# Optimization experiments

Measured on AMD Instinct MI355X. Metric: run time of the kernel, lower is better.

## Reference

```python
import jax, jax.numpy as jnp
import numpy as np

H = 2048          # hidden_size
NH = 32           # num_attention_heads
NKV = 8           # num_key_value_heads
HD = H // NH      # head_dim = 64
ROT = int(HD * 0.25)  # rotary_ndims = 16
THETA = 10000.0


def _rope_cos_sin(seq_len, position_ids):
    # inv_freq over the rotary dims
    inv_freq = 1.0 / (THETA ** (jnp.arange(0, ROT, 2, dtype=jnp.float32) / ROT))
    t = jnp.arange(seq_len, dtype=jnp.float32)
    freqs = jnp.outer(t, inv_freq)              # [S, ROT/2]
    emb = jnp.concatenate([freqs, freqs], -1)   # [S, ROT]
    cos = jnp.cos(emb)[position_ids][:, None]   # [B, 1, Q, ROT]
    sin = jnp.sin(emb)[position_ids][:, None]
    return cos, sin


def _rotate_half(x):
    x1, x2 = jnp.split(x, 2, axis=-1)
    return jnp.concatenate([-x2, x1], axis=-1)


def setup_inputs() -> dict:
    key = jax.random.key(0)
    ks = jax.random.split(key, 5)
    B, S = 2, 2048
    hidden_states = jax.random.normal(ks[0], (B, S, H), jnp.float32)
    # additive causal mask
    neg = jnp.finfo(jnp.float32).min
    causal = jnp.where(jnp.tril(jnp.ones((S, S), bool)), 0.0, neg).astype(jnp.float32)
    attention_mask = jnp.broadcast_to(causal[None, None], (B, 1, S, S))
    position_ids = jnp.broadcast_to(jnp.arange(S, dtype=jnp.int32)[None], (B, S))
    sc = 0.02
    Wq = jax.random.normal(ks[1], (H, H), jnp.float32) * sc
    Wk = jax.random.normal(ks[2], (NKV * HD, H), jnp.float32) * sc
    Wv = jax.random.normal(ks[3], (NKV * HD, H), jnp.float32) * sc
    Wo = jax.random.normal(ks[4], (H, H), jnp.float32) * sc
    return {"hidden_states": hidden_states, "attention_mask": attention_mask,
            "position_ids": position_ids, "Wq": Wq, "Wk": Wk, "Wv": Wv, "Wo": Wo}


def reference(hidden_states, attention_mask, position_ids, Wq, Wk, Wv, Wo):
    B, S, _ = hidden_states.shape
    q = (hidden_states @ Wq.T).reshape(B, S, NH, HD).transpose(0, 2, 1, 3)    # [B,NH,S,HD]
    k = (hidden_states @ Wk.T).reshape(B, S, NKV, HD).transpose(0, 2, 1, 3)   # [B,NKV,S,HD]
    v = (hidden_states @ Wv.T).reshape(B, S, NKV, HD).transpose(0, 2, 1, 3)

    cos, sin = _rope_cos_sin(S, position_ids)  # [B,1,S,ROT]
    q_rot, q_pass = q[..., :ROT], q[..., ROT:]
    k_rot, k_pass = k[..., :ROT], k[..., ROT:]
    q_rot = q_rot * cos + _rotate_half(q_rot) * sin
    k_rot = k_rot * cos + _rotate_half(k_rot) * sin
    q = jnp.concatenate([q_rot, q_pass], -1)
    k = jnp.concatenate([k_rot, k_pass], -1)

    # GQA without materializing repeated K/V: group Q heads per KV head
    G = NH // NKV
    qg = q.reshape(B, NKV, G, S, HD)
    scores = jnp.einsum('bhgqd,bhkd->bhgqk', qg, k) / np.sqrt(HD)
    scores = scores.reshape(B, NH, S, S) + attention_mask
    probs = jax.nn.softmax(scores.astype(jnp.float32), axis=-1).astype(q.dtype)
    out = jnp.einsum('bhgqk,bhkd->bhgqd', probs.reshape(B, NKV, G, S, S), v)
    out = out.reshape(B, NH, S, HD).transpose(0, 2, 1, 3).reshape(B, S, H)
    return out @ Wo.T
```

## Files before the change

### kernel.cpp

```cpp
#include <hip/hip_runtime.h>

typedef unsigned short u16;
typedef short s16x8 __attribute__((ext_vector_type(8)));
typedef u16 u16x8 __attribute__((ext_vector_type(8)));
typedef u16 u16x4 __attribute__((ext_vector_type(4)));
typedef float f32x4 __attribute__((ext_vector_type(4)));
typedef __bf16 bf16x8 __attribute__((ext_vector_type(8)));
typedef __bf16 bf16x4 __attribute__((ext_vector_type(4)));

#define B_ 2
#define S_ 2048
#define H_ 2048
#define NH_ 32
#define NKV_ 8
#define HD_ 64
#define LDQ_ 3072
#define NTOK (B_ * S_)
#define SC_ 0.18033688011112042f

__device__ __forceinline__ u16 f2bf(float f) {
  unsigned u = __float_as_uint(f);
  u += 0x7fffu + ((u >> 16) & 1u);
  return (u16)(u >> 16);
}
__device__ __forceinline__ float bf2f(u16 h) {
  return __uint_as_float(((unsigned)h) << 16);
}

__device__ __forceinline__ void gload16(const void* g, void* l) {
  __builtin_amdgcn_global_load_lds(
      (const __attribute__((address_space(1))) unsigned int*)g,
      (__attribute__((address_space(3))) unsigned int*)l, 16, 0, 0);
}

__device__ __forceinline__ f32x4 mfma16(s16x8 a, s16x8 b, f32x4 c) {
  return __builtin_amdgcn_mfma_f32_16x16x32_bf16(
      __builtin_bit_cast(bf16x8, a), __builtin_bit_cast(bf16x8, b), c, 0, 0, 0);
}

__global__ __launch_bounds__(256) void cvt_all(const float* __restrict__ hs,
    const float* __restrict__ wq, const float* __restrict__ wk,
    const float* __restrict__ wv, const float* __restrict__ wo,
    u16* __restrict__ xbf, u16* __restrict__ wqkv, u16* __restrict__ wob,
    float* __restrict__ tab) {
  int i = blockIdx.x * 256 + threadIdx.x;
  if (i >= 2359296) {
    int t = i - 2359296;
    if (t < S_ * 8) {
      int p = t >> 3, k = t & 7;
      float inv = powf(10000.0f, -(float)k * 0.125f);
      float ang = (float)p * inv;
      tab[p * 16 + k] = cosf(ang);
      tab[p * 16 + 8 + k] = sinf(ang);
    }
    return;
  }
  const float* s; u16* d; int j;
  if (i < 1048576)      { s = hs; d = xbf;            j = i; }
  else if (i < 1572864) { s = wq; d = wqkv;           j = i - 1048576; }
  else if (i < 1703936) { s = wk; d = wqkv + 4194304; j = i - 1572864; }
  else if (i < 1835008) { s = wv; d = wqkv + 5242880; j = i - 1703936; }
  else                  { s = wo; d = wob;            j = i - 1835008; }
  const float4* sp = (const float4*)s + (size_t)j * 2;
  float4 a = sp[0], b = sp[1];
  u16x8 o;
  o[0] = f2bf(a.x); o[1] = f2bf(a.y); o[2] = f2bf(a.z); o[3] = f2bf(a.w);
  o[4] = f2bf(b.x); o[5] = f2bf(b.y); o[6] = f2bf(b.z); o[7] = f2bf(b.w);
  *((u16x8*)d + j) = o;
}

__device__ __forceinline__ void store_c(u16* p, float v) { *p = f2bf(v); }
__device__ __forceinline__ void store_c(float* p, float v) { *p = v; }

template <typename OutT, bool SCQ, bool ROPE, bool WRV>
__global__ __launch_bounds__(256, 3) void gemm_bt(const u16* __restrict__ A,
                                                  const u16* __restrict__ Bw,
                                                  OutT* __restrict__ C,
                                                  u16* __restrict__ Vt,
                                                  const float* __restrict__ tab,
                                                  int M, int N, int K) {
  __shared__ u16 lds[2 * 128 * 64];
  u16* ldsA = lds;
  u16* ldsB = lds + 128 * 64;
  const int tid = threadIdx.x;
  const int lane = tid & 63;
  const int wave = tid >> 6;
  const int wm = (wave & 1) * 64;
  const int wn = (wave >> 1) * 64;
  const int m0 = blockIdx.y * 128;
  const int n0 = blockIdx.x * 128;
  const int l15 = lane & 15;
  const int quad = lane >> 4;
  const int xs = l15 & 7;

  f32x4 acc[4][4];
#pragma unroll
  for (int i = 0; i < 4; ++i)
#pragma unroll
    for (int j = 0; j < 4; ++j) acc[i][j] = {0.f, 0.f, 0.f, 0.f};

  const u16* Ab = A + (size_t)m0 * K;
  const u16* Bb = Bw + (size_t)n0 * K;

  for (int k0 = 0; k0 < K; k0 += 64) {
    __syncthreads();
#pragma unroll
    for (int it = 0; it < 4; ++it) {
      int c = it * 256 + tid;
      int row = c >> 3;
      int sw = ((c & 7) ^ (row & 7)) * 8;
      gload16(Ab + (size_t)row * K + k0 + sw, ldsA + (size_t)c * 8);
      gload16(Bb + (size_t)row * K + k0 + sw, ldsB + (size_t)c * 8);
    }
    __syncthreads();
#pragma unroll
    for (int ks = 0; ks < 2; ++ks) {
      int slot = ((ks * 4 + quad) ^ xs) * 8;
      s16x8 af[4], bfr[4];
#pragma unroll
      for (int i = 0; i < 4; ++i)
        af[i] = *(const s16x8*)(ldsA + (size_t)(wm + i * 16 + l15) * 64 + slot);
#pragma unroll
      for (int j = 0; j < 4; ++j)
        bfr[j] = *(const s16x8*)(ldsB + (size_t)(wn + j * 16 + l15) * 64 + slot);
#pragma unroll
      for (int i = 0; i < 4; ++i)
#pragma unroll
        for (int j = 0; j < 4; ++j)
          acc[i][j] = mfma16(af[i], bfr[j], acc[i][j]);
    }
  }
  if (WRV && n0 >= 2560) {
#pragma unroll
    for (int i = 0; i < 4; ++i) {
      int row = m0 + wm + i * 16 + quad * 4;
      int bb = row >> 11;
      int s = row & (S_ - 1);
#pragma unroll
      for (int j = 0; j < 4; ++j) {
        int colb = n0 + wn + j * 16 - 2560;
        int kvh = colb >> 6;
        int d = (colb & 63) + l15;
        u16x4 w;
#pragma unroll
        for (int r = 0; r < 4; ++r) w[r] = f2bf(acc[i][j][r]);
        *(u16x4*)(Vt + ((size_t)(bb * 8 + kvh) * 64 + d) * (size_t)S_ + s) = w;
      }
    }
    return;
  }
  const float qs = (SCQ && n0 < 2048) ? SC_ : 1.0f;
  const bool doRope = ROPE && (n0 + wn < 2560);
#pragma unroll
  for (int i = 0; i < 4; ++i) {
    int row = m0 + wm + i * 16 + quad * 4;
#pragma unroll
    for (int j = 0; j < 4; ++j) {
      int col = n0 + wn + j * 16 + l15;
#pragma unroll
      for (int r = 0; r < 4; ++r) {
        float v = acc[i][j][r] * qs;
        if (ROPE) {
          if (j == 0 && doRope) {
            int p = (row + r) & (S_ - 1);
            float c = tab[p * 16 + (l15 & 7)];
            float s = tab[p * 16 + 8 + (l15 & 7)];
            float px = __shfl_xor(v, 8);
            v = (l15 < 8) ? (v * c - px * s) : (v * c + px * s);
          }
        }
        store_c(C + (size_t)(row + r) * N + col, v);
      }
    }
  }
}

template <bool DIAG>
__device__ __forceinline__ void softmax_pack(const f32x4* sc, u16* prow,
                                             int q2, int xs, int sb, int qg) {
#pragma unroll
  for (int nt = 0; nt < 4; ++nt) {
    f32x4 p;
#pragma unroll
    for (int r = 0; r < 4; ++r) {
      float e = __builtin_amdgcn_exp2f(sc[nt][r]);
      if (DIAG) e = (sb + nt * 16 + r > qg) ? 0.0f : e;
      p[r] = e;
    }
    bf16x4 w;
    w[0] = (__bf16)p[0]; w[1] = (__bf16)p[1];
    w[2] = (__bf16)p[2]; w[3] = (__bf16)p[3];
    *(bf16x4*)(prow + (((nt * 2) | q2) ^ xs) * 8) = w;
  }
}

__global__ __launch_bounds__(256, 3) void flash_attn(const u16* __restrict__ QKV,
                                                     const u16* __restrict__ Vt,
                                                     u16* __restrict__ O) {
  __shared__ u16 Kl2[2][64 * 64];
  __shared__ u16 Vl2[2][64 * 64];
  __shared__ u16 Pb[4][16 * 64];
  const int h = blockIdx.x;
  const int b = blockIdx.y;
  const int qt = 15 - (int)blockIdx.z;
  const int kvh = h >> 2;
  const int tid = threadIdx.x;
  const int lane = tid & 63;
  const int wave = tid >> 6;
  const int l15 = lane & 15;
  const int quad = lane >> 4;
  const int xs = l15 & 7;

  const u16* Qb = QKV + (size_t)b * S_ * LDQ_ + h * 64;
  const u16* Kb = QKV + (size_t)b * S_ * LDQ_ + 2048 + kvh * 64;
  const u16* Vb = Vt + (size_t)(b * 8 + kvh) * HD_ * S_;

  const int row0w = qt * 128 + wave * 32;

  s16x8 qf[2][2];
#pragma unroll
  for (int g = 0; g < 2; ++g) {
    int qrow = row0w + g * 16 + l15;
#pragma unroll
    for (int ks = 0; ks < 2; ++ks)
      qf[g][ks] = *(const s16x8*)(Qb + (size_t)qrow * LDQ_ + ks * 32 + quad * 8);
  }

  s16x8 ones;
#pragma unroll
  for (int i = 0; i < 8; ++i) ones[i] = (short)0x3F80;

  f32x4 acc_o[2][4];
#pragma unroll
  for (int g = 0; g < 2; ++g)
#pragma unroll
    for (int nt = 0; nt < 4; ++nt) acc_o[g][nt] = {0.f, 0.f, 0.f, 0.f};
  f32x4 acc_l[2] = {{0.f, 0.f, 0.f, 0.f}, {0.f, 0.f, 0.f, 0.f}};

  const int r0 = tid >> 3, c0 = tid & 7;
  const int ch0 = c0 * 8;
  const int r1 = r0 + 32;
  const int ss = (c0 ^ (r0 & 7)) * 8;

  const int nkt = 2 * qt + 2;

  u16* Pw = Pb[wave] + l15 * 64 + (quad & 1) * 4;
  const int q2 = quad >> 1;
  const u16* Pr0 = Pb[wave] + l15 * 64 + ((quad ^ xs) * 8);
  const u16* Pr1 = Pb[wave] + l15 * 64 + (((quad + 4) ^ xs) * 8);

  u16x8 kr0, kr1, vr0, vr1;
  kr0 = *(const u16x8*)(Kb + (size_t)r0 * LDQ_ + ch0);
  kr1 = *(const u16x8*)(Kb + (size_t)r1 * LDQ_ + ch0);
  vr0 = *(const u16x8*)(Vb + (size_t)r0 * S_ + ch0);
  vr1 = *(const u16x8*)(Vb + (size_t)r1 * S_ + ch0);

  for (int kt = 0; kt < nkt; ++kt) {
    u16* Kl = Kl2[kt & 1];
    u16* Vl = Vl2[kt & 1];
    *(u16x8*)(Kl + r0 * 64 + ss) = kr0;
    *(u16x8*)(Kl + r1 * 64 + ss) = kr1;
    *(u16x8*)(Vl + r0 * 64 + ss) = vr0;
    *(u16x8*)(Vl + r1 * 64 + ss) = vr1;
    __syncthreads();
    if (kt + 1 < nkt) {
      int kb = (kt + 1) * 64;
      kr0 = *(const u16x8*)(Kb + (size_t)(kb + r0) * LDQ_ + ch0);
      kr1 = *(const u16x8*)(Kb + (size_t)(kb + r1) * LDQ_ + ch0);
      vr0 = *(const u16x8*)(Vb + (size_t)r0 * S_ + kb + ch0);
      vr1 = *(const u16x8*)(Vb + (size_t)r1 * S_ + kb + ch0);
    }
    if (kt * 64 <= row0w + 31) {
      const int sl0 = (quad ^ xs) * 8;
      const int sl1 = sl0 ^ 32;
      f32x4 sc[2][4];
      __builtin_amdgcn_s_setprio(1);
#pragma unroll
      for (int nt = 0; nt < 4; ++nt) {
        const u16* kp = Kl + (nt * 16 + l15) * 64;
        s16x8 k0 = *(const s16x8*)(kp + sl0);
        s16x8 k1 = *(const s16x8*)(kp + sl1);
        f32x4 z = {0.f, 0.f, 0.f, 0.f};
        sc[0][nt] = mfma16(k1, qf[0][1], mfma16(k0, qf[0][0], z));
        sc[1][nt] = mfma16(k1, qf[1][1], mfma16(k0, qf[1][0], z));
      }
      __builtin_amdgcn_s_setprio(0);
      const int sb = kt * 64 + quad * 4;
      s16x8 pf[2][2];
#pragma unroll
      for (int g = 0; g < 2; ++g) {
        const int row0 = row0w + g * 16;
        if (kt * 64 + 63 > row0)
          softmax_pack<true>(sc[g], Pw, q2, xs, sb, row0 + l15);
        else
          softmax_pack<false>(sc[g], Pw, q2, xs, sb, row0 + l15);
        pf[g][0] = *(const s16x8*)(Pr0);
        pf[g][1] = *(const s16x8*)(Pr1);
      }
      __builtin_amdgcn_s_setprio(1);
#pragma unroll
      for (int nt = 0; nt < 4; ++nt) {
        const u16* vp = Vl + (nt * 16 + l15) * 64;
        s16x8 v0 = *(const s16x8*)(vp + sl0);
        s16x8 v1 = *(const s16x8*)(vp + sl1);
        acc_o[0][nt] = mfma16(pf[0][1], v1, mfma16(pf[0][0], v0, acc_o[0][nt]));
        acc_o[1][nt] = mfma16(pf[1][1], v1, mfma16(pf[1][0], v0, acc_o[1][nt]));
      }
      acc_l[0] = mfma16(pf[0][1], ones, mfma16(pf[0][0], ones, acc_l[0]));
      acc_l[1] = mfma16(pf[1][1], ones, mfma16(pf[1][0], ones, acc_l[1]));
      __builtin_amdgcn_s_setprio(0);
    }
  }
#pragma unroll
  for (int g = 0; g < 2; ++g) {
#pragma unroll
    for (int r = 0; r < 4; ++r) {
      float inv = 1.0f / acc_l[g][r];
      int row = row0w + g * 16 + quad * 4 + r;
      size_t obase = ((size_t)b * S_ + row) * (size_t)H_ + h * 64;
#pragma unroll
      for (int nt = 0; nt < 4; ++nt)
        O[obase + nt * 16 + l15] = f2bf(acc_o[g][nt][r] * inv);
    }
  }
}

extern "C" void kernel_launch(void* const* d_in, const int* in_sizes, int n_in,
                              void* d_out, int out_size, void* d_ws, size_t ws_size,
                              hipStream_t stream) {
  const float* hs = (const float*)d_in[0];
  const float* Wq = (const float*)d_in[3];
  const float* Wk = (const float*)d_in[4];
  const float* Wv = (const float*)d_in[5];
  const float* Wo = (const float*)d_in[6];
  float* out = (float*)d_out;

  if (ws_size < 67239936) return;

  char* ws = (char*)d_ws;
  u16* Xbf   = (u16*)(ws);
  u16* Wqkv  = (u16*)(ws + 16777216);
  u16* Wob   = (u16*)(ws + 29360128);
  u16* Cqkv  = (u16*)(ws + 37748736);
  u16* Vt    = (u16*)(ws + 62914560);
  float* tab = (float*)(ws + 67108864);
  u16* O     = Xbf;

  cvt_all<<<9280, 256, 0, stream>>>(hs, Wq, Wk, Wv, Wo, Xbf, Wqkv, Wob, tab);
  gemm_bt<u16, true, true, true><<<dim3(24, 32), 256, 0, stream>>>(
      Xbf, Wqkv, Cqkv, Vt, tab, 4096, 3072, 2048);
  flash_attn<<<dim3(32, 2, 16), 256, 0, stream>>>(Cqkv, Vt, O);
  gemm_bt<float, false, false, false><<<dim3(16, 32), 256, 0, stream>>>(
      O, Wob, out, nullptr, nullptr, 4096, 2048, 2048);
}
```

Before: 285.5 us.

## Triple-buffer GEMM LDS tiles with async prefetch two stages ahead

The GEMM main loop moves from a single-buffered 64-wide K tile with two barriers per iteration to a three-stage ring of 32-wide K tiles. Global-to-LDS loads for tile t+2 are issued before computing tile t, and explicit vmcnt waits replace the second barrier. The LDS swizzle is adapted to the 32-element row, and MFMA sections are wrapped in s_setprio. The intent is to hide global load latency behind compute, at the cost of more barriers per unit of K, a larger LDS footprint (48KB) that may lower occupancy, and reliance on the gload16 instruction count matching the vmcnt(4) value.

```diff
diff --git a/kernel.cpp b/kernel.cpp
--- a/kernel.cpp
+++ b/kernel.cpp
@@ -79,9 +79,7 @@
                                                   u16* __restrict__ Vt,
                                                   const float* __restrict__ tab,
                                                   int M, int N, int K) {
-  __shared__ u16 lds[2 * 128 * 64];
-  u16* ldsA = lds;
-  u16* ldsB = lds + 128 * 64;
+  __shared__ u16 lds[3 * 8192];
   const int tid = threadIdx.x;
   const int lane = tid & 63;
   const int wave = tid >> 6;
@@ -91,7 +89,6 @@
   const int n0 = blockIdx.x * 128;
   const int l15 = lane & 15;
   const int quad = lane >> 4;
-  const int xs = l15 & 7;
 
   f32x4 acc[4][4];
 #pragma unroll
@@ -101,34 +98,53 @@
 
   const u16* Ab = A + (size_t)m0 * K;
   const u16* Bb = Bw + (size_t)n0 * K;
-
-  for (int k0 = 0; k0 < K; k0 += 64) {
-    __syncthreads();
-#pragma unroll
-    for (int it = 0; it < 4; ++it) {
+  const int NT = K >> 5;
+
+  auto stage = [&](int t) {
+    u16* buf = lds + (t % 3) * 8192;
+    const int k0 = t << 5;
+#pragma unroll
+    for (int it = 0; it < 2; ++it) {
       int c = it * 256 + tid;
-      int row = c >> 3;
-      int sw = ((c & 7) ^ (row & 7)) * 8;
-      gload16(Ab + (size_t)row * K + k0 + sw, ldsA + (size_t)c * 8);
-      gload16(Bb + (size_t)row * K + k0 + sw, ldsB + (size_t)c * 8);
-    }
-    __syncthreads();
-#pragma unroll
-    for (int ks = 0; ks < 2; ++ks) {
-      int slot = ((ks * 4 + quad) ^ xs) * 8;
-      s16x8 af[4], bfr[4];
-#pragma unroll
-      for (int i = 0; i < 4; ++i)
-        af[i] = *(const s16x8*)(ldsA + (size_t)(wm + i * 16 + l15) * 64 + slot);
+      int row = c >> 2;
+      int sw = ((c & 3) ^ ((row >> 1) & 3)) * 8;
+      gload16(Ab + (size_t)row * K + k0 + sw, buf + (size_t)c * 8);
+      gload16(Bb + (size_t)row * K + k0 + sw, buf + 4096 + (size_t)c * 8);
+    }
+  };
+
+  stage(0);
+  stage(1);
+
+  for (int t = 0; t < NT; ++t) {
+    if (t + 1 < NT)
+      asm volatile("s_waitcnt vmcnt(4) lgkmcnt(0)" ::: "memory");
+    else
+      asm volatile("s_waitcnt vmcnt(0) lgkmcnt(0)" ::: "memory");
+    __builtin_amdgcn_s_barrier();
+    if (t + 2 < NT) stage(t + 2);
+    const u16* bufA = lds + (t % 3) * 8192;
+    const u16* bufB = bufA + 4096;
+    s16x8 af[4], bfr[4];
+#pragma unroll
+    for (int i = 0; i < 4; ++i) {
+      int row = wm + i * 16 + l15;
+      af[i] = *(const s16x8*)(bufA + (size_t)row * 32 +
+                              ((quad ^ ((row >> 1) & 3)) * 8));
+    }
+#pragma unroll
+    for (int j = 0; j < 4; ++j) {
+      int row = wn + j * 16 + l15;
+      bfr[j] = *(const s16x8*)(bufB + (size_t)row * 32 +
+                               ((quad ^ ((row >> 1) & 3)) * 8));
+    }
+    __builtin_amdgcn_s_setprio(1);
+#pragma unroll
+    for (int i = 0; i < 4; ++i)
 #pragma unroll
       for (int j = 0; j < 4; ++j)
-        bfr[j] = *(const s16x8*)(ldsB + (size_t)(wn + j * 16 + l15) * 64 + slot);
-#pragma unroll
-      for (int i = 0; i < 4; ++i)
-#pragma unroll
-        for (int j = 0; j < 4; ++j)
-          acc[i][j] = mfma16(af[i], bfr[j], acc[i][j]);
-    }
+        acc[i][j] = mfma16(af[i], bfr[j], acc[i][j]);
+    __builtin_amdgcn_s_setprio(0);
   }
   if (WRV && n0 >= 2560) {
 #pragma unroll
```

New measurement: 289.7 us. No clear change (+1.5%).
